# Kernel tuning notes

Hardware: AMD Instinct MI355X
Metric: run time of the kernel (lower is better)

The kernel has to match this reference:

```python
import jax, jax.numpy as jnp
import numpy as np

WINDOW = 8
HEADS = 16
HIDDEN = 256
EMBED = HIDDEN * WINDOW          # 2048
HEAD_DIM = EMBED // HEADS        # 128
BATCH = 8
SEQ = 4096                       # multiple of WINDOW
GROUP = SEQ // WINDOW            # 512


def _indices():
    # index_one[i*g + j] = j*w + i  (residue-class grouping permutation)
    i = np.arange(WINDOW)
    j = np.arange(GROUP)
    index_one = (j[None, :] * WINDOW + i[:, None]).reshape(-1)
    # index_two[i*w + k] = k*g + i  (inverse-style interleave permutation)
    index_two = (np.arange(WINDOW)[None, :] * GROUP + np.arange(GROUP)[:, None]).reshape(-1)
    return jnp.asarray(index_one), jnp.asarray(index_two)


def _attention(M, Wq, Wk, Wv, fc_w, fc_b):
    # M: [N, g, E] with E = heads*head_dim
    N, L, E = M.shape
    x = M.reshape(N, L, HEADS, HEAD_DIM)
    q = jnp.einsum('nlhd,ed->nlhe', x, Wq)
    k = jnp.einsum('nlhd,ed->nlhe', x, Wk)
    v = jnp.einsum('nlhd,ed->nlhe', x, Wv)
    energy = jnp.einsum('nqhd,nkhd->nhqk', q, k)
    attn = jax.nn.softmax(energy / jnp.sqrt(jnp.float32(EMBED)), axis=-1)
    out = jnp.einsum('nhqk,nkhd->nqhd', attn, v).reshape(N, L, E)
    return out @ fc_w.T + fc_b


def setup_inputs() -> dict:
    key = jax.random.key(0)
    ks = jax.random.split(key, 6)
    s = 0.02
    return {
        'M': jax.random.normal(ks[0], (BATCH, SEQ, HIDDEN), jnp.float32),
        'Wq': jax.random.normal(ks[1], (HEAD_DIM, HEAD_DIM), jnp.float32) * s,
        'Wk': jax.random.normal(ks[2], (HEAD_DIM, HEAD_DIM), jnp.float32) * s,
        'Wv': jax.random.normal(ks[3], (HEAD_DIM, HEAD_DIM), jnp.float32) * s,
        'fc_w': jax.random.normal(ks[4], (EMBED, EMBED), jnp.float32) * s,
        'fc_b': jax.random.normal(ks[5], (EMBED,), jnp.float32) * s,
        'device': 0,
    }


def reference(M, Wq, Wk, Wv, fc_w, fc_b, device):
    del device  # unused, mirrors torch signature
    index_one, index_two = _indices()
    N, S, H = M.shape
    w, g = WINDOW, GROUP
    for b in range(w):
        idx = (index_one - b) % S
        M = M[:, idx]                                             # gather permute
        # segmentation step 1: [N, w*g, H] -> [N, g, w*H]
        M = M.reshape(N, w, g, H).transpose(0, 2, 1, 3).reshape(N, g, w * H)
        M = _attention(M, Wq, Wk, Wv, fc_w, fc_b)
        # segmentation step 2: [N, g, w*H] -> [N, w*g, H]
        M = M.reshape(N, g, w, H).transpose(0, 2, 1, 3).reshape(N, w * g, H)
        # index_two rotated once per iteration after the first -> roll by -b
        M = M[:, jnp.roll(index_two, -b)]
    return M[:, :S]
```

## Files before the change

### kernel.cpp

```cpp
#include <hip/hip_runtime.h>
#include <stdint.h>

typedef unsigned short u16;
typedef unsigned int u32;
typedef __bf16 bf16x8 __attribute__((ext_vector_type(8)));
typedef float f32x4 __attribute__((ext_vector_type(4)));
typedef float f32x16 __attribute__((ext_vector_type(16)));
typedef u16 u16x4 __attribute__((ext_vector_type(4)));
typedef u16 u16x8 __attribute__((ext_vector_type(8)));

#define MFMA16(a, b, c) __builtin_amdgcn_mfma_f32_16x16x32_bf16(a, b, c, 0, 0, 0)
#define MFMA32(a, b, c) __builtin_amdgcn_mfma_f32_32x32x16_bf16(a, b, c, 0, 0, 0)

__device__ __forceinline__ u16 f2bf(float f) {
  u32 u = __builtin_bit_cast(u32, f);
  u += 0x7FFFu + ((u >> 16) & 1u);
  return (u16)(u >> 16);
}

__device__ __forceinline__ bf16x8 ld16(const u16* p) {
  return __builtin_bit_cast(bf16x8, *(const uint4*)p);
}

__device__ __forceinline__ void gl_lds(const u16* src, u16* lds) {
  __builtin_amdgcn_global_load_lds(
      (const __attribute__((address_space(1))) u32*)src,
      (__attribute__((address_space(3))) u32*)lds, 16, 0, 0);
}

__global__ __launch_bounds__(256) void convert_weights(
    const float* __restrict__ Wq, const float* __restrict__ Wk,
    const float* __restrict__ Wv, const float* __restrict__ fcw,
    u16* __restrict__ wq_b, u16* __restrict__ wk_b, u16* __restrict__ wv_b,
    u16* __restrict__ fcw_b) {
  int bx = blockIdx.x, tid = threadIdx.x;
  if (bx < 4096) {
    int i = (bx * 256 + tid) * 4;
    float4 f = *(const float4*)&fcw[i];
    u16x4 o = {f2bf(f.x), f2bf(f.y), f2bf(f.z), f2bf(f.w)};
    *(u16x4*)&fcw_b[i] = o;
  } else {
    int i = ((bx - 4096) * 256 + tid) * 4;
    const float sc = 0.022097086912079612f;
    float4 q = *(const float4*)&Wq[i];
    u16x4 oq = {f2bf(q.x * sc), f2bf(q.y * sc), f2bf(q.z * sc), f2bf(q.w * sc)};
    *(u16x4*)&wq_b[i] = oq;
    float4 k = *(const float4*)&Wk[i];
    u16x4 ok = {f2bf(k.x), f2bf(k.y), f2bf(k.z), f2bf(k.w)};
    *(u16x4*)&wk_b[i] = ok;
    float4 v = *(const float4*)&Wv[i];
    u16x4 ov = {f2bf(v.x), f2bf(v.y), f2bf(v.z), f2bf(v.w)};
    *(u16x4*)&wv_b[i] = ov;
  }
}

__global__ __launch_bounds__(384) void qkv_kernel(
    const float* __restrict__ src, const u16* __restrict__ wq,
    const u16* __restrict__ wk, const u16* __restrict__ wvw,
    u16* __restrict__ Q, u16* __restrict__ K, u16* __restrict__ Vt, int bsh) {
  __shared__ u16 X[64 * 136];
  int jt = blockIdx.x, h = blockIdx.y, n = blockIdx.z;
  int tid = threadIdx.x;
  int i0 = h >> 1, c0 = (h & 1) * 128;
  for (int it = 0; it < 3; ++it) {
    int c = tid + it * 384;
    if (c < 1024) {
      int row = c >> 4, seg = c & 15;
      int j = jt * 64 + row;
      int pos = (8 * j + i0 - bsh) & 4095;
      const float* g = src + ((size_t)n * 4096 + pos) * 256 + c0 + seg * 8;
      float4 f0 = *(const float4*)g;
      float4 f1 = *(const float4*)(g + 4);
      u16x8 v = {f2bf(f0.x), f2bf(f0.y), f2bf(f0.z), f2bf(f0.w),
                 f2bf(f1.x), f2bf(f1.y), f2bf(f1.z), f2bf(f1.w)};
      *(u16x8*)&X[row * 136 + seg * 8] = v;
    }
  }
  __syncthreads();
  int wv = tid >> 6, ln = tid & 63;
  int mat = wv >> 1;
  int cbase = (wv & 1) * 64;
  const u16* W = (mat == 0) ? wq : (mat == 1) ? wk : wvw;
  int lr = ln & 15, lg = ln >> 4;
  f32x4 acc[4][4] = {};
#pragma unroll
  for (int kt = 0; kt < 4; ++kt) {
    bf16x8 a[4], b[4];
#pragma unroll
    for (int mt = 0; mt < 4; ++mt)
      a[mt] = ld16(&X[(mt * 16 + lr) * 136 + kt * 32 + lg * 8]);
#pragma unroll
    for (int nc = 0; nc < 4; ++nc)
      b[nc] = ld16(&W[(cbase + nc * 16 + lr) * 128 + kt * 32 + lg * 8]);
#pragma unroll
    for (int mt = 0; mt < 4; ++mt)
#pragma unroll
      for (int nc = 0; nc < 4; ++nc)
        acc[mt][nc] = MFMA16(a[mt], b[nc], acc[mt][nc]);
  }
  size_t nh = (size_t)(n * 16 + h);
  if (mat < 2) {
    u16* dst = (mat == 0 ? Q : K) + nh * 512 * 128;
#pragma unroll
    for (int mt = 0; mt < 4; ++mt)
#pragma unroll
      for (int nc = 0; nc < 4; ++nc) {
        int col = cbase + nc * 16 + lr;
        int jb = jt * 64 + mt * 16 + lg * 4;
#pragma unroll
        for (int r = 0; r < 4; ++r)
          dst[(size_t)(jb + r) * 128 + col] = f2bf(acc[mt][nc][r]);
      }
  } else {
    u16* dst = Vt + nh * 128 * 512;
#pragma unroll
    for (int mt = 0; mt < 4; ++mt)
#pragma unroll
      for (int nc = 0; nc < 4; ++nc) {
        int col = cbase + nc * 16 + lr;
        int jb = jt * 64 + mt * 16 + lg * 4;
        u16x4 pk = {f2bf(acc[mt][nc][0]), f2bf(acc[mt][nc][1]),
                    f2bf(acc[mt][nc][2]), f2bf(acc[mt][nc][3])};
        *(u16x4*)&dst[(size_t)col * 512 + jb] = pk;
      }
  }
}

__global__ __launch_bounds__(256, 2) void attn_kernel(
    const u16* __restrict__ Q, const u16* __restrict__ K,
    const u16* __restrict__ Vt, u16* __restrict__ O) {
  __shared__ u16 KL[2][64 * 128];
  __shared__ u16 VL[2][128 * 64];
  int flat = blockIdx.x;
  int xcd = flat & 7, idx = flat >> 3;
  int gl = idx & 15, qt = idx >> 4;
  int g = xcd | (gl << 3);
  int h = g & 15, n = g >> 4;
  int tid = threadIdx.x, wv = tid >> 6, ln = tid & 63;
  int l31 = ln & 31, hh = ln >> 5;
  size_t nh = (size_t)(n * 16 + h);
  int q0 = qt * 128 + wv * 32;
  const u16* Qb = Q + ((size_t)nh * 512 + q0) * 128;
  const u16* Kb = K + (size_t)nh * 512 * 128;
  const u16* Vb = Vt + (size_t)nh * 128 * 512;

  bf16x8 qf[8];
#pragma unroll
  for (int kt = 0; kt < 8; ++kt)
    qf[kt] = ld16(&Qb[l31 * 128 + kt * 16 + hh * 8]);

  int l16 = ln & 15, l8 = ln & 7;
  int rK[4], cK[4], rV[4], cV[4];
#pragma unroll
  for (int i = 0; i < 4; ++i) {
    int s = wv * 4 + i;
    rK[i] = 4 * s + (ln >> 4);
    cK[i] = (l16 ^ (rK[i] & 15)) * 8;
    rV[i] = 8 * s + (ln >> 3);
    cV[i] = (l8 ^ (rV[i] & 7)) * 8;
  }

#pragma unroll
  for (int i = 0; i < 4; ++i) {
    int s = wv * 4 + i;
    gl_lds(&Kb[(size_t)rK[i] * 128 + cK[i]], &KL[0][s * 512]);
    gl_lds(&Vb[(size_t)rV[i] * 512 + 0 * 64 + cV[i]], &VL[0][s * 512]);
  }
  __syncthreads();

  f32x16 o[4] = {};
  float m = -1e30f, l = 0.f;

  for (int kv = 0; kv < 8; ++kv) {
    int cur = kv & 1;
    if (kv < 7) {
      int nxt = cur ^ 1;
      const u16* kp = Kb + (size_t)(kv + 1) * 64 * 128;
#pragma unroll
      for (int i = 0; i < 4; ++i) {
        int s = wv * 4 + i;
        gl_lds(&kp[(size_t)rK[i] * 128 + cK[i]], &KL[nxt][s * 512]);
        gl_lds(&Vb[(size_t)rV[i] * 512 + (kv + 1) * 64 + cV[i]], &VL[nxt][s * 512]);
      }
    }
    f32x16 s[2] = {};
#pragma unroll
    for (int kb = 0; kb < 2; ++kb)
#pragma unroll
      for (int kt = 0; kt < 8; ++kt) {
        int row = kb * 32 + l31;
        int slot = (2 * kt + hh) ^ (row & 15);
        bf16x8 a = ld16(&KL[cur][row * 128 + slot * 8]);
        s[kb] = MFMA32(a, qf[kt], s[kb]);
      }
    float mx[8];
#pragma unroll
    for (int i = 0; i < 8; ++i)
      mx[i] = fmaxf(fmaxf(s[0][2 * i], s[0][2 * i + 1]),
                    fmaxf(s[1][2 * i], s[1][2 * i + 1]));
    float pm = fmaxf(fmaxf(fmaxf(mx[0], mx[1]), fmaxf(mx[2], mx[3])),
                     fmaxf(fmaxf(mx[4], mx[5]), fmaxf(mx[6], mx[7])));
    pm = fmaxf(pm, __shfl_xor(pm, 32));
    if (!__all(pm <= m + 8.f)) {
      float nm = fmaxf(m, pm);
      float al = __expf(m - nm);
      l *= al;
      m = nm;
#pragma unroll
      for (int r = 0; r < 16; ++r) {
        int qr = (r & 3) + 8 * (r >> 2) + 4 * hh;
        float av = __shfl(al, (ln & 32) | qr, 64);
        o[0][r] *= av; o[1][r] *= av; o[2][r] *= av; o[3][r] *= av;
      }
    }
#pragma unroll
    for (int kb = 0; kb < 2; ++kb)
#pragma unroll
      for (int r = 0; r < 16; ++r) s[kb][r] = __expf(s[kb][r] - m);
    float sm[8];
#pragma unroll
    for (int i = 0; i < 8; ++i)
      sm[i] = (s[0][2 * i] + s[0][2 * i + 1]) + (s[1][2 * i] + s[1][2 * i + 1]);
    float rs = ((sm[0] + sm[1]) + (sm[2] + sm[3])) +
               ((sm[4] + sm[5]) + (sm[6] + sm[7]));
    rs += __shfl_xor(rs, 32);
    l += rs;
    bf16x8 pa[4];
#pragma unroll
    for (int ks = 0; ks < 4; ++ks) {
      const int kb = ks >> 1, r0 = 8 * (ks & 1);
      u32 wA, wB, wC, wD;
      asm("v_cvt_pk_bf16_f32 %0, %1, %2" : "=v"(wA) : "v"(s[kb][r0 + 0]), "v"(s[kb][r0 + 1]));
      asm("v_cvt_pk_bf16_f32 %0, %1, %2" : "=v"(wB) : "v"(s[kb][r0 + 2]), "v"(s[kb][r0 + 3]));
      asm("v_cvt_pk_bf16_f32 %0, %1, %2" : "=v"(wC) : "v"(s[kb][r0 + 4]), "v"(s[kb][r0 + 5]));
      asm("v_cvt_pk_bf16_f32 %0, %1, %2" : "=v"(wD) : "v"(s[kb][r0 + 6]), "v"(s[kb][r0 + 7]));
      asm("v_permlane32_swap_b32 %0, %1" : "+v"(wA), "+v"(wC));
      asm("v_permlane32_swap_b32 %0, %1" : "+v"(wB), "+v"(wD));
      uint4 ww = {wA, wB, wC, wD};
      pa[ks] = __builtin_bit_cast(bf16x8, ww);
    }
#pragma unroll
    for (int ks = 0; ks < 4; ++ks)
#pragma unroll
      for (int nb = 0; nb < 4; ++nb) {
        int row = nb * 32 + l31;
        int slot = (2 * ks + hh) ^ (row & 7);
        bf16x8 bv = ld16(&VL[cur][row * 64 + slot * 8]);
        o[nb] = MFMA32(pa[ks], bv, o[nb]);
      }
    if (kv < 7) __syncthreads();
  }
  float inv = 1.f / l;
#pragma unroll
  for (int r = 0; r < 16; ++r) {
    int qr = (r & 3) + 8 * (r >> 2) + 4 * hh;
    float iv = __shfl(inv, (ln & 32) | qr, 64);
    int row = q0 + qr;
    u16* dst = O + ((size_t)n * 512 + row) * 2048 + h * 128;
    dst[0 * 32 + l31] = f2bf(o[0][r] * iv);
    dst[1 * 32 + l31] = f2bf(o[1][r] * iv);
    dst[2 * 32 + l31] = f2bf(o[2][r] * iv);
    dst[3 * 32 + l31] = f2bf(o[3][r] * iv);
  }
}

__global__ __launch_bounds__(256) void fc_kernel(
    const u16* __restrict__ A, const u16* __restrict__ Bw,
    const float* __restrict__ bias, float* __restrict__ dout, int bsh) {
  __shared__ u16 Al[128 * 32];
  __shared__ u16 Bl[128 * 32];
  int bn = blockIdx.x, bm = blockIdx.y;
  int tid = threadIdx.x, wv = tid >> 6, ln = tid & 63;
  int lr = ln & 15, lg = ln >> 4;
  int R0 = bm * 128, C0 = bn * 128;
  int wr = (wv & 1) * 64, wc = (wv >> 1) * 64;
  int lrow = ln >> 2, lseg = ln & 3;
  f32x4 acc[4][4] = {};
  for (int ks = 0; ks < 64; ++ks) {
    int k0 = ks * 32;
#pragma unroll
    for (int ch = wv; ch < 8; ch += 4) {
      const u16* ga = A + (size_t)(R0 + ch * 16 + lrow) * 2048 + k0 + lseg * 8;
      gl_lds(ga, &Al[ch * 512]);
      const u16* gb = Bw + (size_t)(C0 + ch * 16 + lrow) * 2048 + k0 + lseg * 8;
      gl_lds(gb, &Bl[ch * 512]);
    }
    __syncthreads();
    bf16x8 a[4], b[4];
#pragma unroll
    for (int mt = 0; mt < 4; ++mt)
      a[mt] = ld16(&Al[(wr + mt * 16 + lr) * 32 + lg * 8]);
#pragma unroll
    for (int nc = 0; nc < 4; ++nc)
      b[nc] = ld16(&Bl[(wc + nc * 16 + lr) * 32 + lg * 8]);
#pragma unroll
    for (int mt = 0; mt < 4; ++mt)
#pragma unroll
      for (int nc = 0; nc < 4; ++nc)
        acc[mt][nc] = MFMA16(a[mt], b[nc], acc[mt][nc]);
    __syncthreads();
  }
#pragma unroll
  for (int nc = 0; nc < 4; ++nc) {
    int e = C0 + wc + nc * 16 + lr;
    float bv = bias[e];
    int i = e >> 8, cc = e & 255;
#pragma unroll
    for (int mt = 0; mt < 4; ++mt)
#pragma unroll
      for (int r = 0; r < 4; ++r) {
        int row = R0 + wr + mt * 16 + lg * 4 + r;
        int nn = row >> 9, j = row & 511;
        int pos = (8 * j + i - bsh) & 4095;
        dout[((size_t)nn * 4096 + pos) * 256 + cc] = acc[mt][nc][r] + bv;
      }
  }
}

extern "C" void kernel_launch(void* const* d_in, const int* in_sizes, int n_in,
                              void* d_out, int out_size, void* d_ws, size_t ws_size,
                              hipStream_t stream) {
  const float* M = (const float*)d_in[0];
  const float* Wq = (const float*)d_in[1];
  const float* Wk = (const float*)d_in[2];
  const float* Wv = (const float*)d_in[3];
  const float* fcw = (const float*)d_in[4];
  const float* fcb = (const float*)d_in[5];
  float* out = (float*)d_out;
  char* ws = (char*)d_ws;
  u16* wq_b = (u16*)(ws + (0 << 10));
  u16* wk_b = (u16*)(ws + (32 << 10));
  u16* wv_b = (u16*)(ws + (64 << 10));
  u16* fcw_b = (u16*)(ws + (128 << 10));
  u16* Qb = (u16*)(ws + ((size_t)16 << 20));
  u16* Kb = (u16*)(ws + ((size_t)32 << 20));
  u16* Vtb = (u16*)(ws + ((size_t)48 << 20));
  u16* Ab = (u16*)(ws + ((size_t)64 << 20));

  convert_weights<<<4112, 256, 0, stream>>>(Wq, Wk, Wv, fcw, wq_b, wk_b, wv_b, fcw_b);
  for (int b = 0; b < 8; ++b) {
    const float* src = (b == 0) ? M : out;
    qkv_kernel<<<dim3(8, 16, 8), 384, 0, stream>>>(src, wq_b, wk_b, wv_b, Qb, Kb, Vtb, b);
    attn_kernel<<<512, 256, 0, stream>>>(Qb, Kb, Vtb, Ab);
    fc_kernel<<<dim3(16, 32), 256, 0, stream>>>(Ab, fcw_b, fcb, out, b);
  }
}
```

Baseline: 810.0 us.

## Double-buffer FC GEMM with swizzled LDS, merge QKV head pairs, add MFMA priority

The FC GEMM moves to a double-buffered 64-wide K tile with an XOR-swizzled LDS layout. It issues global-to-LDS prefetches ahead of compute, waits on vmcnt, and raises wave priority around the MFMA blocks. The QKV kernel now handles both heads of a window offset in one 768-thread block, so each source row is read once as a full 256-float row instead of two half rows. Attention gets s_setprio hints around its two MFMA phases. The intent is to hide load latency and cut redundant global reads, at the cost of more LDS per block, which may limit occupancy.

```diff
diff --git a/kernel.cpp b/kernel.cpp
--- a/kernel.cpp
+++ b/kernel.cpp
@@ -54,32 +54,29 @@
   }
 }
 
-__global__ __launch_bounds__(384) void qkv_kernel(
+__global__ __launch_bounds__(768) void qkv_kernel(
     const float* __restrict__ src, const u16* __restrict__ wq,
     const u16* __restrict__ wk, const u16* __restrict__ wvw,
     u16* __restrict__ Q, u16* __restrict__ K, u16* __restrict__ Vt, int bsh) {
-  __shared__ u16 X[64 * 136];
-  int jt = blockIdx.x, h = blockIdx.y, n = blockIdx.z;
+  __shared__ u16 X[64 * 264];
+  int jt = blockIdx.x, i0 = blockIdx.y, n = blockIdx.z;
   int tid = threadIdx.x;
-  int i0 = h >> 1, c0 = (h & 1) * 128;
-  for (int it = 0; it < 3; ++it) {
-    int c = tid + it * 384;
-    if (c < 1024) {
-      int row = c >> 4, seg = c & 15;
-      int j = jt * 64 + row;
-      int pos = (8 * j + i0 - bsh) & 4095;
-      const float* g = src + ((size_t)n * 4096 + pos) * 256 + c0 + seg * 8;
-      float4 f0 = *(const float4*)g;
-      float4 f1 = *(const float4*)(g + 4);
-      u16x8 v = {f2bf(f0.x), f2bf(f0.y), f2bf(f0.z), f2bf(f0.w),
-                 f2bf(f1.x), f2bf(f1.y), f2bf(f1.z), f2bf(f1.w)};
-      *(u16x8*)&X[row * 136 + seg * 8] = v;
+#pragma unroll
+  for (int r = 0; r < 6; ++r) {
+    int idx = tid + r * 768;
+    if (idx < 4096) {
+      int row = idx >> 6, c4 = idx & 63;
+      int pos = (8 * (jt * 64 + row) + i0 - bsh) & 4095;
+      float4 f = *(const float4*)&src[((size_t)n * 4096 + pos) * 256 + c4 * 4];
+      u16x4 v = {f2bf(f.x), f2bf(f.y), f2bf(f.z), f2bf(f.w)};
+      *(u16x4*)&X[row * 264 + c4 * 4] = v;
     }
   }
   __syncthreads();
-  int wv = tid >> 6, ln = tid & 63;
-  int mat = wv >> 1;
-  int cbase = (wv & 1) * 64;
+  int wvid = tid >> 6, ln = tid & 63;
+  int mat = wvid >> 2, hc = wvid & 3;
+  int hh = hc >> 1, cb = (hc & 1) * 64;
+  int h = i0 * 2 + hh, xc = hh * 128;
   const u16* W = (mat == 0) ? wq : (mat == 1) ? wk : wvw;
   int lr = ln & 15, lg = ln >> 4;
   f32x4 acc[4][4] = {};
@@ -88,10 +85,10 @@
     bf16x8 a[4], b[4];
 #pragma unroll
     for (int mt = 0; mt < 4; ++mt)
-      a[mt] = ld16(&X[(mt * 16 + lr) * 136 + kt * 32 + lg * 8]);
+      a[mt] = ld16(&X[(mt * 16 + lr) * 264 + xc + kt * 32 + lg * 8]);
 #pragma unroll
     for (int nc = 0; nc < 4; ++nc)
-      b[nc] = ld16(&W[(cbase + nc * 16 + lr) * 128 + kt * 32 + lg * 8]);
+      b[nc] = ld16(&W[(cb + nc * 16 + lr) * 128 + kt * 32 + lg * 8]);
 #pragma unroll
     for (int mt = 0; mt < 4; ++mt)
 #pragma unroll
@@ -105,7 +102,7 @@
     for (int mt = 0; mt < 4; ++mt)
 #pragma unroll
       for (int nc = 0; nc < 4; ++nc) {
-        int col = cbase + nc * 16 + lr;
+        int col = cb + nc * 16 + lr;
         int jb = jt * 64 + mt * 16 + lg * 4;
 #pragma unroll
         for (int r = 0; r < 4; ++r)
@@ -117,7 +114,7 @@
     for (int mt = 0; mt < 4; ++mt)
 #pragma unroll
       for (int nc = 0; nc < 4; ++nc) {
-        int col = cbase + nc * 16 + lr;
+        int col = cb + nc * 16 + lr;
         int jb = jt * 64 + mt * 16 + lg * 4;
         u16x4 pk = {f2bf(acc[mt][nc][0]), f2bf(acc[mt][nc][1]),
                     f2bf(acc[mt][nc][2]), f2bf(acc[mt][nc][3])};
@@ -184,6 +181,7 @@
       }
     }
     f32x16 s[2] = {};
+    __builtin_amdgcn_s_setprio(1);
 #pragma unroll
     for (int kb = 0; kb < 2; ++kb)
 #pragma unroll
@@ -193,6 +191,7 @@
         bf16x8 a = ld16(&KL[cur][row * 128 + slot * 8]);
         s[kb] = MFMA32(a, qf[kt], s[kb]);
       }
+    __builtin_amdgcn_s_setprio(0);
     float mx[8];
 #pragma unroll
     for (int i = 0; i < 8; ++i)
@@ -239,6 +238,7 @@
       uint4 ww = {wA, wB, wC, wD};
       pa[ks] = __builtin_bit_cast(bf16x8, ww);
     }
+    __builtin_amdgcn_s_setprio(1);
 #pragma unroll
     for (int ks = 0; ks < 4; ++ks)
 #pragma unroll
@@ -248,6 +248,7 @@
         bf16x8 bv = ld16(&VL[cur][row * 64 + slot * 8]);
         o[nb] = MFMA32(pa[ks], bv, o[nb]);
       }
+    __builtin_amdgcn_s_setprio(0);
     if (kv < 7) __syncthreads();
   }
   float inv = 1.f / l;
@@ -264,41 +265,72 @@
   }
 }
 
-__global__ __launch_bounds__(256) void fc_kernel(
+__global__ __launch_bounds__(256, 2) void fc_kernel(
     const u16* __restrict__ A, const u16* __restrict__ Bw,
     const float* __restrict__ bias, float* __restrict__ dout, int bsh) {
-  __shared__ u16 Al[128 * 32];
-  __shared__ u16 Bl[128 * 32];
+  __shared__ u16 AL[2][128 * 64];
+  __shared__ u16 BL[2][128 * 64];
   int bn = blockIdx.x, bm = blockIdx.y;
   int tid = threadIdx.x, wv = tid >> 6, ln = tid & 63;
   int lr = ln & 15, lg = ln >> 4;
   int R0 = bm * 128, C0 = bn * 128;
   int wr = (wv & 1) * 64, wc = (wv >> 1) * 64;
-  int lrow = ln >> 2, lseg = ln & 3;
+  const u16 *gAsrc[4], *gBsrc[4];
+  int srow[4];
+#pragma unroll
+  for (int i = 0; i < 4; ++i) {
+    int r = i * 32 + wv * 8 + (ln >> 3);
+    int cs = ((ln & 7) ^ (r & 7)) * 8;
+    gAsrc[i] = A + (size_t)(R0 + r) * 2048 + cs;
+    gBsrc[i] = Bw + (size_t)(C0 + r) * 2048 + cs;
+    srow[i] = i * 32 + wv * 8;
+  }
+  int aoff[4][2], boff[4][2];
+#pragma unroll
+  for (int i = 0; i < 4; ++i) {
+    int ra = wr + i * 16 + lr, rb = wc + i * 16 + lr;
+#pragma unroll
+    for (int kk = 0; kk < 2; ++kk) {
+      aoff[i][kk] = ra * 64 + (((kk * 4 + lg) ^ (ra & 7)) * 8);
+      boff[i][kk] = rb * 64 + (((kk * 4 + lg) ^ (rb & 7)) * 8);
+    }
+  }
   f32x4 acc[4][4] = {};
-  for (int ks = 0; ks < 64; ++ks) {
-    int k0 = ks * 32;
-#pragma unroll
-    for (int ch = wv; ch < 8; ch += 4) {
-      const u16* ga = A + (size_t)(R0 + ch * 16 + lrow) * 2048 + k0 + lseg * 8;
-      gl_lds(ga, &Al[ch * 512]);
-      const u16* gb = Bw + (size_t)(C0 + ch * 16 + lrow) * 2048 + k0 + lseg * 8;
-      gl_lds(gb, &Bl[ch * 512]);
-    }
-    __syncthreads();
-    bf16x8 a[4], b[4];
-#pragma unroll
-    for (int mt = 0; mt < 4; ++mt)
-      a[mt] = ld16(&Al[(wr + mt * 16 + lr) * 32 + lg * 8]);
-#pragma unroll
-    for (int nc = 0; nc < 4; ++nc)
-      b[nc] = ld16(&Bl[(wc + nc * 16 + lr) * 32 + lg * 8]);
-#pragma unroll
-    for (int mt = 0; mt < 4; ++mt)
-#pragma unroll
-      for (int nc = 0; nc < 4; ++nc)
-        acc[mt][nc] = MFMA16(a[mt], b[nc], acc[mt][nc]);
-    __syncthreads();
+#pragma unroll
+  for (int i = 0; i < 4; ++i) {
+    gl_lds(gAsrc[i], &AL[0][srow[i] * 64]);
+    gl_lds(gBsrc[i], &BL[0][srow[i] * 64]);
+  }
+  for (int t = 0; t < 32; ++t) {
+    int cur = t & 1, nx = cur ^ 1;
+    if (t < 31) {
+      int k0 = (t + 1) * 64;
+#pragma unroll
+      for (int i = 0; i < 4; ++i) {
+        gl_lds(gAsrc[i] + k0, &AL[nx][srow[i] * 64]);
+        gl_lds(gBsrc[i] + k0, &BL[nx][srow[i] * 64]);
+      }
+      asm volatile("s_waitcnt vmcnt(8)" ::: "memory");
+    } else {
+      asm volatile("s_waitcnt vmcnt(0)" ::: "memory");
+    }
+    __builtin_amdgcn_s_barrier();
+#pragma unroll
+    for (int kk = 0; kk < 2; ++kk) {
+      bf16x8 a[4], b[4];
+#pragma unroll
+      for (int i = 0; i < 4; ++i) a[i] = ld16(&AL[cur][aoff[i][kk]]);
+#pragma unroll
+      for (int i = 0; i < 4; ++i) b[i] = ld16(&BL[cur][boff[i][kk]]);
+      __builtin_amdgcn_s_setprio(1);
+#pragma unroll
+      for (int mt = 0; mt < 4; ++mt)
+#pragma unroll
+        for (int nc = 0; nc < 4; ++nc)
+          acc[mt][nc] = MFMA16(a[mt], b[nc], acc[mt][nc]);
+      __builtin_amdgcn_s_setprio(0);
+    }
+    if (t < 31) __builtin_amdgcn_s_barrier();
   }
 #pragma unroll
   for (int nc = 0; nc < 4; ++nc) {
@@ -340,7 +372,7 @@
   convert_weights<<<4112, 256, 0, stream>>>(Wq, Wk, Wv, fcw, wq_b, wk_b, wv_b, fcw_b);
   for (int b = 0; b < 8; ++b) {
     const float* src = (b == 0) ? M : out;
-    qkv_kernel<<<dim3(8, 16, 8), 384, 0, stream>>>(src, wq_b, wk_b, wv_b, Qb, Kb, Vtb, b);
+    qkv_kernel<<<dim3(8, 8, 8), 768, 0, stream>>>(src, wq_b, wk_b, wv_b, Qb, Kb, Vtb, b);
     attn_kernel<<<512, 256, 0, stream>>>(Qb, Kb, Vtb, Ab);
     fc_kernel<<<dim3(16, 32), 256, 0, stream>>>(Ab, fcw_b, fcb, out, b);
   }
```

New measurement: 736.4 us. 1.1x faster.
